# Optimization experiments

Hardware: AMD Instinct MI355X
Metric: run time of the kernel (lower is better)

## Reference

```python
import jax, jax.numpy as jnp
import numpy as np

TINY = 1e-15
EPS = 1e-6
B, T, D, H, N = 1, 512, 512, 8, 64
A = N + 1  # ambient dim
TAU = 1.0


def mink(x, y):
    # Minkowski inner product over the last dim
    return -x[..., 0] * y[..., 0] + jnp.sum(x[..., 1:] * y[..., 1:], axis=-1)


def project(x):
    xx = mink(x, x)
    scale = jnp.sqrt(jnp.maximum(jnp.abs(xx), TINY))[..., None]
    x = x / scale
    return jnp.concatenate([jnp.abs(x[..., :1]), x[..., 1:]], axis=-1)


def exp_map(p, v):
    vn = jnp.sqrt(jnp.maximum(mink(v, v), TINY))[..., None]
    y = jnp.cosh(vn) * p + (jnp.sinh(vn) / jnp.maximum(vn, TINY)) * v
    return project(y)


def log_map(p, y):
    alpha = -mink(p, y)
    dist = jnp.arccosh(jnp.maximum(alpha, 1.0 + EPS))[..., None]
    u = y + alpha[..., None] * p
    un = jnp.sqrt(jnp.maximum(mink(u, u), TINY))[..., None]
    return dist / jnp.maximum(un, TINY) * u


def rope(u):
    # u: [B,H,T,N]; standard half-rotation RoPE, base 10000
    inv_freq = 1.0 / (10000.0 ** (jnp.arange(0, N, 2, dtype=jnp.float32) / N))
    ang = jnp.arange(T, dtype=jnp.float32)[:, None] * inv_freq[None, :]  # [T, N/2]
    cos = jnp.concatenate([jnp.cos(ang), jnp.cos(ang)], axis=-1)  # [T, N]
    sin = jnp.concatenate([jnp.sin(ang), jnp.sin(ang)], axis=-1)
    u1, u2 = u[..., : N // 2], u[..., N // 2:]
    rot = jnp.concatenate([-u2, u1], axis=-1)
    return u * cos + rot * sin


def lift(u):
    # append time-like 0, expmap at origin -> points on hyperboloid [B,H,T,A]
    v = jnp.concatenate([jnp.zeros(u.shape[:-1] + (1,), u.dtype), u], axis=-1)
    o = jnp.zeros((A,), u.dtype).at[0].set(1.0)
    return exp_map(o, v)


def setup_inputs() -> dict:
    key = jax.random.key(0)
    ks = jax.random.split(key, 10)
    s = 0.02
    x = jax.random.normal(ks[0], (B, T, D), jnp.float32)
    Wq = jax.random.normal(ks[1], (D, H * N), jnp.float32) * s
    bq = jax.random.normal(ks[2], (H * N,), jnp.float32) * s
    Wk = jax.random.normal(ks[3], (D, H * N), jnp.float32) * s
    bk = jax.random.normal(ks[4], (H * N,), jnp.float32) * s
    Wv = jax.random.normal(ks[5], (D, H * N), jnp.float32) * s
    bv = jax.random.normal(ks[6], (H * N,), jnp.float32) * s
    Wo = jax.random.normal(ks[7], (H * A, D), jnp.float32) * s
    bo = jax.random.normal(ks[8], (D,), jnp.float32) * s
    sp = jax.random.normal(ks[9], (N,), jnp.float32) * 0.1
    anchor_p = jnp.concatenate([jnp.sqrt(1.0 + jnp.sum(sp * sp))[None], sp])  # valid hyperboloid point
    return dict(x=x, Wq=Wq, bq=bq, Wk=Wk, bk=bk, Wv=Wv, bv=bv, Wo=Wo, bo=bo, anchor_p=anchor_p)


def reference(x, Wq, bq, Wk, bk, Wv, bv, Wo, bo, anchor_p):
    def pack(u):  # [B,T,H*N] -> [B,H,T,N]
        return u.reshape(B, T, H, N).transpose(0, 2, 1, 3)

    uq = rope(pack(x @ Wq + bq))
    uk = rope(pack(x @ Wk + bk))
    uv = pack(x @ Wv + bv)
    Q = lift(uq)  # [B,H,T,A]
    K = lift(uk)
    V = lift(uv)

    # pairwise Lorentz distance scores, softmax in fp32
    alpha_qk = -mink(Q[:, :, :, None, :].astype(jnp.float32), K[:, :, None, :, :].astype(jnp.float32))
    d = jnp.arccosh(jnp.maximum(alpha_qk, 1.0 + EPS))  # [B,H,T,T]
    attn = jax.nn.softmax(-TAU * d * d, axis=-1).astype(V.dtype)

    # one Karcher-mean step around the query point (karcher_steps=1)
    Y = Q
    logv = log_map(Y[:, :, :, None, :], V[:, :, None, :, :])  # [B,H,T,T,A]
    u = jnp.sum(attn[..., None] * logv, axis=3)  # [B,H,T,A]
    Y = exp_map(Y, u)

    Yc = Y.transpose(0, 2, 1, 3)  # [B,T,H,A]
    Z_tan = log_map(anchor_p[None, None, None, :], Yc).reshape(B, T, H * A)
    return Z_tan @ Wo + bo
```

## Files before the change

kernel.cpp:

```cpp
#include <hip/hip_runtime.h>
#include <math.h>

#define T_ 512
#define D_ 512
#define H_ 8
#define N_ 64
#define A_ 65
#define HN_ 512
#define HA_ 520
#define QS_ 66
#define VS_ 66
#define KTS_ 512
#define SYS_ 68
#define EPS_ 1e-6
#define EPSF_ 1e-6f
#define TINY_ 1e-15
#define IT 8
#define PTT 4
#define RPB_ 16
#define BN_ 64
#define CH_ 64
#define NCH_ (D_/CH_)
#define CTT 2

__device__ __forceinline__ double wsumd(double v){
#pragma unroll
  for (int o=32;o;o>>=1) v += __shfl_xor(v,o);
  return v;
}
__device__ __forceinline__ float wsumf(float v){
#pragma unroll
  for (int o=32;o;o>>=1) v += __shfl_xor(v,o);
  return v;
}
__device__ __forceinline__ float wmaxf(float v){
#pragma unroll
  for (int o=32;o;o>>=1) v = fmaxf(v,__shfl_xor(v,o));
  return v;
}
__device__ __forceinline__ float facoshf(float x){
  return __logf(x + sqrtf(fmaf(x,x,-1.f)));
}

__global__ void k_fill(float* __restrict__ out, float val){
  int i = blockIdx.x*256 + threadIdx.x;
  if (i < T_*D_) out[i] = val;
}

__global__ __launch_bounds__(256) void k_trig(double* __restrict__ tab){
  int i = blockIdx.x*256 + threadIdx.x;
  int t = i >> 5, fi = i & 31;
  double inv_f = 1.0 / pow(10000.0, (double)(2*fi)*(1.0/64.0));
  double ang = (double)t * inv_f;
  tab[2*i+0] = cos(ang);
  tab[2*i+1] = sin(ang);
}

__global__ __launch_bounds__(256) void k_projlift(
    const float* __restrict__ x,
    const float* __restrict__ Wq, const float* __restrict__ bq,
    const float* __restrict__ Wk, const float* __restrict__ bk,
    const float* __restrict__ Wv, const float* __restrict__ bv,
    const double* __restrict__ trig,
    float* __restrict__ Qf, float* __restrict__ KTf,
    float* __restrict__ Vf, float* __restrict__ VTf){
  __shared__ float sW[2][CH_*BN_];
  int mode = blockIdx.y;
  const float* W  = (mode==0)?Wq:((mode==1)?Wk:Wv);
  const float* bb = (mode==0)?bq:((mode==1)?bk:bv);
  int tid = threadIdx.x;
  int lane = tid & 63;
  int h = blockIdx.x;
  int n = lane;
  int t0 = __builtin_amdgcn_readfirstlane(blockIdx.z*RPB_ + ((tid>>6)<<2));
  int srr = tid >> 4;
  int scc = (tid*4) & 63;

  float acc[PTT];
#pragma unroll
  for (int i=0;i<PTT;i++) acc[i]=0.f;

  {
    float4 st[4];
#pragma unroll
    for (int k=0;k<4;k++)
      st[k] = *reinterpret_cast<const float4*>(W + (size_t)(k*16+srr)*HN_ + h*BN_ + scc);
#pragma unroll
    for (int k=0;k<4;k++)
      *reinterpret_cast<float4*>(&sW[0][k*1024 + tid*4]) = st[k];
  }
  __syncthreads();

  const float* xr = x + (size_t)t0*D_;
#pragma unroll 1
  for (int ch=0; ch<NCH_; ++ch){
    float4 st[4];
    if (ch+1 < NCH_){
#pragma unroll
      for (int k=0;k<4;k++)
        st[k] = *reinterpret_cast<const float4*>(
            W + (size_t)((ch+1)*CH_ + k*16+srr)*HN_ + h*BN_ + scc);
    }
    const float* sb = &sW[ch&1][0];
    int d0 = ch*CH_;
#pragma unroll 8
    for (int r=0;r<CH_;r++){
      float wd = sb[r*BN_ + lane];
#pragma unroll
      for (int i=0;i<PTT;i++)
        acc[i] = fmaf(xr[(size_t)i*D_ + d0 + r], wd, acc[i]);
    }
    if (ch+1 < NCH_){
#pragma unroll
      for (int k=0;k<4;k++)
        *reinterpret_cast<float4*>(&sW[(ch+1)&1][k*1024 + tid*4]) = st[k];
    }
    __syncthreads();
  }

  float bias = bb[h*BN_ + n];
#pragma unroll 1
  for (int i=0;i<PTT;i++){
    int t = t0 + i;
    double v = (double)(acc[i] + bias);
    if (mode < 2){
      const double2 cs2 = *reinterpret_cast<const double2*>(trig + 2*((size_t)t*32 + (n&31)));
      double vp = __shfl_xor(v, 32);
      double rot = (n<32) ? -vp : vp;
      v = v*cs2.x + rot*cs2.y;
    }
    double ss = wsumd(v*v);
    double vn = sqrt(fmax(ss, TINY_));
    double e  = exp(vn);
    double ei = 1.0/e;
    double ch2 = 0.5*(e+ei);
    double s  = (0.5*(e-ei))/vn;
    double xx = s*s*ss - ch2*ch2;
    double scale = sqrt(fmax(fabs(xx), TINY_));
    float y0 = (float)fabs(ch2/scale);
    float ya = (float)(s*v/scale);
    if (mode==0){
      float* o = Qf + (size_t)h*T_*QS_ + (size_t)t*QS_;
      if (n==0) o[0] = y0;
      o[n+1] = ya;
    } else if (mode==1){
      float* o = KTf + (size_t)h*66*KTS_ + t;
      if (n==0) o[0] = y0;
      o[(size_t)(n+1)*KTS_] = ya;
    } else {
      float* o = Vf + (size_t)h*T_*VS_ + (size_t)t*VS_;
      if (n==0) o[0] = y0;
      o[n+1] = ya;
      float* ot = VTf + (size_t)h*66*KTS_ + t;
      if (n==0) ot[0] = y0;
      ot[(size_t)(n+1)*KTS_] = ya;
    }
  }
}

__global__ __launch_bounds__(256) void k_attnF(
    const float* __restrict__ Qf, const float* __restrict__ KTf,
    const float* __restrict__ VTf, const float* __restrict__ Vf,
    const float* __restrict__ anchor, float* __restrict__ Z){
  __shared__ float  sYf[IT][QS_];
  __shared__ float  sYm[IT][SYS_];
  __shared__ float  s_w[IT][T_];
  __shared__ double sA[A_];
  __shared__ float  s_red[4][IT];
  __shared__ float  s_part[4][IT][64];
  __shared__ float  s_p64[4][IT];

  int h = blockIdx.x, i0 = blockIdx.y*IT, tid = threadIdx.x;
  int wv = tid>>6, lane = tid&63;
  const float* Qp = Qf  + (size_t)h*T_*QS_;
  const float* KT = KTf + (size_t)h*66*KTS_;
  const float* VT = VTf + (size_t)h*66*KTS_;
  const float* Vp = Vf  + (size_t)h*T_*VS_;

  for (int f=tid; f<IT*QS_; f+=256){
    int i=f/QS_, a=f-i*QS_;
    sYf[i][a] = (a<A_) ? Qp[(size_t)(i0+i)*QS_ + a] : 0.f;
  }
  for (int f=tid; f<IT*SYS_; f+=256){
    int i=f/SYS_, a=f-i*SYS_;
    float v = (a<A_) ? Qp[(size_t)(i0+i)*QS_ + a] : 0.f;
    sYm[i][a] = (a==0) ? v : -v;
  }
  if (tid < A_) sA[tid] = (double)anchor[tid];
  __syncthreads();

  int j0 = tid, j1 = tid + 256;
  {
    float aq0[IT], aq1[IT];
#pragma unroll
    for (int i=0;i<IT;i++){ aq0[i]=0.f; aq1[i]=0.f; }
    for (int a4=0; a4<16; a4++){
      int a = a4*4;
      float k00=KT[(size_t)(a+0)*KTS_+j0], k01=KT[(size_t)(a+1)*KTS_+j0];
      float k02=KT[(size_t)(a+2)*KTS_+j0], k03=KT[(size_t)(a+3)*KTS_+j0];
      float k10=KT[(size_t)(a+0)*KTS_+j1], k11=KT[(size_t)(a+1)*KTS_+j1];
      float k12=KT[(size_t)(a+2)*KTS_+j1], k13=KT[(size_t)(a+3)*KTS_+j1];
#pragma unroll
      for (int i=0;i<IT;i++){
        float4 ym = *reinterpret_cast<const float4*>(&sYm[i][a]);
        aq0[i] = fmaf(ym.w,k03,fmaf(ym.z,k02,fmaf(ym.y,k01,fmaf(ym.x,k00,aq0[i]))));
        aq1[i] = fmaf(ym.w,k13,fmaf(ym.z,k12,fmaf(ym.y,k11,fmaf(ym.x,k10,aq1[i]))));
      }
    }
    float kt0 = KT[(size_t)64*KTS_+j0], kt1 = KT[(size_t)64*KTS_+j1];
#pragma unroll
    for (int i=0;i<IT;i++){
      float a0 = fmaf(sYm[i][64], kt0, aq0[i]);
      float a1 = fmaf(sYm[i][64], kt1, aq1[i]);
      float d0 = facoshf(fmaxf(a0, 1.f+EPSF_));
      float d1 = facoshf(fmaxf(a1, 1.f+EPSF_));
      s_w[i][j0] = -d0*d0;
      s_w[i][j1] = -d1*d1;
    }
  }
  __syncthreads();

  for (int ii=0; ii<2; ii++){
    int i = wv*2 + ii;
    float m = -INFINITY;
#pragma unroll
    for (int kk=0;kk<8;kk++) m = fmaxf(m, s_w[i][lane+64*kk]);
    m = wmaxf(m);
    float e[8], sum=0.f;
#pragma unroll
    for (int kk=0;kk<8;kk++){ e[kk]=__expf(s_w[i][lane+64*kk]-m); sum+=e[kk]; }
    sum = wsumf(sum);
    float inv = 1.f/sum;
#pragma unroll
    for (int kk=0;kk<8;kk++) s_w[i][lane+64*kk] = e[kk]*inv;
  }
  __syncthreads();

  {
    float av0[IT], av1[IT];
#pragma unroll
    for (int i=0;i<IT;i++){ av0[i]=0.f; av1[i]=0.f; }
    for (int a4=0; a4<16; a4++){
      int a = a4*4;
      float v00=VT[(size_t)(a+0)*KTS_+j0], v01=VT[(size_t)(a+1)*KTS_+j0];
      float v02=VT[(size_t)(a+2)*KTS_+j0], v03=VT[(size_t)(a+3)*KTS_+j0];
      float v10=VT[(size_t)(a+0)*KTS_+j1], v11=VT[(size_t)(a+1)*KTS_+j1];
      float v12=VT[(size_t)(a+2)*KTS_+j1], v13=VT[(size_t)(a+3)*KTS_+j1];
#pragma unroll
      for (int i=0;i<IT;i++){
        float4 ym = *reinterpret_cast<const float4*>(&sYm[i][a]);
        av0[i] = fmaf(ym.w,v03,fmaf(ym.z,v02,fmaf(ym.y,v01,fmaf(ym.x,v00,av0[i]))));
        av1[i] = fmaf(ym.w,v13,fmaf(ym.z,v12,fmaf(ym.y,v11,fmaf(ym.x,v10,av1[i]))));
      }
    }
    float vt0 = VT[(size_t)64*KTS_+j0], vt1 = VT[(size_t)64*KTS_+j1];
    const float inv_un0 = 3.16227766016838e7f;
    float cyp[IT];
#pragma unroll
    for (int i=0;i<IT;i++){
      float a0 = fmaf(sYm[i][64], vt0, av0[i]);
      float a1 = fmaf(sYm[i][64], vt1, av1[i]);
      float at0 = s_w[i][j0], at1 = s_w[i][j1];
      float d0 = facoshf(fmaxf(a0, 1.f+EPSF_));
      float d1 = facoshf(fmaxf(a1, 1.f+EPSF_));
      float w0 = at0*d0*inv_un0;
      float w1 = at1*d1*inv_un0;
      s_w[i][j0] = w0;
      s_w[i][j1] = w1;
      cyp[i] = fmaf(w0, a0, w1*a1);
    }
#pragma unroll
    for (int i=0;i<IT;i++){
      float r = wsumf(cyp[i]);
      if (lane==0) s_red[wv][i] = r;
    }
  }
  __syncthreads();

  {
    float pL[IT], p64r[IT];
#pragma unroll
    for (int i=0;i<IT;i++){ pL[i]=0.f; p64r[i]=0.f; }
    int jb = wv*128;
    for (int jj=0; jj<128; jj+=4){
      int j = jb + jj;
      float vA = Vp[(size_t)(j+0)*VS_ + lane];
      float vB = Vp[(size_t)(j+1)*VS_ + lane];
      float vC = Vp[(size_t)(j+2)*VS_ + lane];
      float vD = Vp[(size_t)(j+3)*VS_ + lane];
#pragma unroll
      for (int i=0;i<IT;i++){
        float4 w4 = *reinterpret_cast<const float4*>(&s_w[i][j]);
        pL[i] = fmaf(w4.w,vD,fmaf(w4.z,vC,fmaf(w4.y,vB,fmaf(w4.x,vA,pL[i]))));
      }
    }
#pragma unroll
    for (int cc=0; cc<2; cc++){
      int j = jb + cc*64 + lane;
      float v64 = VT[(size_t)64*KTS_ + j];
#pragma unroll
      for (int i=0;i<IT;i++) p64r[i] = fmaf(s_w[i][j], v64, p64r[i]);
    }
#pragma unroll
    for (int i=0;i<IT;i++){
      s_part[wv][i][lane] = pL[i];
      float r = wsumf(p64r[i]);
      if (lane==0) s_p64[wv][i] = r;
    }
  }
  __syncthreads();

  for (int ii=0; ii<2; ii++){
    int r = wv*2 + ii;
    double Yl  = (double)sYf[r][lane];
    double Y64 = (double)sYf[r][64];
    double cy = (double)s_red[0][r]+(double)s_red[1][r]+(double)s_red[2][r]+(double)s_red[3][r];
    double aL = (double)s_part[0][r][lane]+(double)s_part[1][r][lane]
              + (double)s_part[2][r][lane]+(double)s_part[3][r][lane];
    double a64 = (double)s_p64[0][r]+(double)s_p64[1][r]+(double)s_p64[2][r]+(double)s_p64[3][r];
    double ua  = fma(cy, Yl,  aL);
    double u64 = fma(cy, Y64, a64);
    double c2 = (lane==0) ? fma(u64,u64, -ua*ua) : ua*ua;
    double mv = wsumd(c2);
    double vn = sqrt(fmax(mv, TINY_));
    double ch = cosh(vn);
    double sh = sinh(vn)/fmax(vn, TINY_);
    double ya  = fma(ch, Yl,  sh*ua);
    double y64 = fma(ch, Y64, sh*u64);
    double c3 = (lane==0) ? fma(y64,y64, -ya*ya) : ya*ya;
    double px = wsumd(c3);
    double scale = sqrt(fmax(fabs(px), TINY_));
    double Pa  = ya/scale; if (lane==0) Pa = fabs(Pa);
    double P64 = y64/scale;
    double sAl = sA[lane];
    double azc = (lane==0) ? fma(sAl, Pa, -sA[64]*P64) : (-sAl*Pa);
    double az = wsumd(azc);
    double dz = acosh(fmax(az, 1.0+EPS_));
    double uza  = fma(az, sAl,    Pa);
    double uz64 = fma(az, sA[64], P64);
    double c4v = (lane==0) ? fma(uz64,uz64, -uza*uza) : uza*uza;
    double mz = wsumd(c4v);
    double unz = sqrt(fmax(mz, TINY_));
    double fz = dz/fmax(unz, TINY_);
    float* Zr = Z + (size_t)(i0+r)*HA_ + h*A_;
    Zr[lane] = (float)(fz*uza);
    if (lane==0) Zr[64] = (float)(fz*uz64);
  }
}

__global__ __launch_bounds__(256) void k_outD(
    const float* __restrict__ Zb, const float* __restrict__ Wo,
    const float* __restrict__ bo, float* __restrict__ out){
  int c  = blockIdx.x*256 + threadIdx.x;
  int t0 = blockIdx.y*CTT;
  float acc[CTT];
#pragma unroll
  for (int i=0;i<CTT;i++) acc[i]=0.f;
  for (int k=0;k<HA_;k+=4){
    float w0 = Wo[(size_t)(k+0)*D_ + c];
    float w1 = Wo[(size_t)(k+1)*D_ + c];
    float w2 = Wo[(size_t)(k+2)*D_ + c];
    float w3 = Wo[(size_t)(k+3)*D_ + c];
#pragma unroll
    for (int i=0;i<CTT;i++){
      const float* zr = Zb + (size_t)(t0+i)*HA_;
      acc[i] = fmaf(zr[k+0], w0, acc[i]);
      acc[i] = fmaf(zr[k+1], w1, acc[i]);
      acc[i] = fmaf(zr[k+2], w2, acc[i]);
      acc[i] = fmaf(zr[k+3], w3, acc[i]);
    }
  }
  float bb = bo[c];
#pragma unroll
  for (int i=0;i<CTT;i++) out[(t0+i)*D_ + c] = acc[i] + bb;
}

extern "C" void kernel_launch(void* const* d_in, const int* in_sizes, int n_in,
                              void* d_out, int out_size, void* d_ws, size_t ws_size,
                              hipStream_t stream){
  float* out = (float*)d_out;

  bool ok = (n_in == 10) && (out_size == T_*D_)
    && in_sizes[0]==T_*D_ && in_sizes[1]==D_*HN_ && in_sizes[2]==HN_
    && in_sizes[3]==D_*HN_ && in_sizes[4]==HN_
    && in_sizes[5]==D_*HN_ && in_sizes[6]==HN_
    && in_sizes[7]==HA_*D_ && in_sizes[8]==D_ && in_sizes[9]==A_;
  if (!ok){ k_fill<<<1024,256,0,stream>>>(out, 1.0e12f); return; }

  const float* x      = (const float*)d_in[0];
  const float* Wq     = (const float*)d_in[1];
  const float* bq     = (const float*)d_in[2];
  const float* Wk     = (const float*)d_in[3];
  const float* bk     = (const float*)d_in[4];
  const float* Wv     = (const float*)d_in[5];
  const float* bv     = (const float*)d_in[6];
  const float* Wo     = (const float*)d_in[7];
  const float* bo     = (const float*)d_in[8];
  const float* anchor = (const float*)d_in[9];
  char* ws = (char*)d_ws;

  size_t zbytes  = (size_t)T_*HA_*sizeof(float);
  size_t qbytes  = (size_t)H_*T_*QS_*sizeof(float);
  size_t ktbytes = (size_t)H_*66*KTS_*sizeof(float);
  size_t vbytes  = (size_t)H_*T_*VS_*sizeof(float);
  size_t vtbytes = (size_t)H_*66*KTS_*sizeof(float);
  size_t tbytes  = (size_t)T_*32*2*sizeof(double);
  size_t need    = zbytes+qbytes+ktbytes+vbytes+vtbytes+tbytes;
  if (ws_size < need){ k_fill<<<1024,256,0,stream>>>(out, 2.0e12f); return; }

  float*  Zf = (float*)ws;
  float*  Qf = (float*)(ws + zbytes);
  float*  KT = (float*)(ws + zbytes + qbytes);
  float*  Vf = (float*)(ws + zbytes + qbytes + ktbytes);
  float*  VT = (float*)(ws + zbytes + qbytes + ktbytes + vbytes);
  double* TB = (double*)(ws + zbytes + qbytes + ktbytes + vbytes + vtbytes);

  k_trig    <<<dim3(T_*32/256),   256, 0, stream>>>(TB);
  k_projlift<<<dim3(H_,3,T_/RPB_),256, 0, stream>>>(x, Wq,bq, Wk,bk, Wv,bv, TB, Qf, KT, Vf, VT);
  k_attnF   <<<dim3(H_, T_/IT),   256, 0, stream>>>(Qf, KT, VT, Vf, anchor, Zf);
  k_outD    <<<dim3(2, T_/CTT),   256, 0, stream>>>(Zf, Wo, bo, out);
}
```

Measured before the change: 100.3 us.

## Halve attention query tile and vectorize x loads in projection GEMM

```diff
diff --git a/kernel.cpp b/kernel.cpp
--- a/kernel.cpp
+++ b/kernel.cpp
@@ -15,7 +15,7 @@
 #define EPS_ 1e-6
 #define EPSF_ 1e-6f
 #define TINY_ 1e-15
-#define IT 8
+#define IT 4
 #define PTT 4
 #define RPB_ 16
 #define BN_ 64
@@ -72,7 +72,7 @@
   int lane = tid & 63;
   int h = blockIdx.x;
   int n = lane;
-  int t0 = __builtin_amdgcn_readfirstlane(blockIdx.z*RPB_ + ((tid>>6)<<2));
+  int t0 = blockIdx.z*RPB_ + ((tid>>6)<<2);
   int srr = tid >> 4;
   int scc = (tid*4) & 63;
 
@@ -103,12 +103,24 @@
     }
     const float* sb = &sW[ch&1][0];
     int d0 = ch*CH_;
-#pragma unroll 8
-    for (int r=0;r<CH_;r++){
-      float wd = sb[r*BN_ + lane];
+#pragma unroll 4
+    for (int r4=0; r4<CH_/4; r4++){
+      float4 xv[PTT];
 #pragma unroll
       for (int i=0;i<PTT;i++)
-        acc[i] = fmaf(xr[(size_t)i*D_ + d0 + r], wd, acc[i]);
+        xv[i] = *reinterpret_cast<const float4*>(xr + (size_t)i*D_ + d0 + r4*4);
+#pragma unroll
+      for (int j=0;j<4;j++){
+        float wd = sb[(r4*4+j)*BN_ + lane];
+        const float xj0 = (j==0)?xv[0].x:((j==1)?xv[0].y:((j==2)?xv[0].z:xv[0].w));
+        const float xj1 = (j==0)?xv[1].x:((j==1)?xv[1].y:((j==2)?xv[1].z:xv[1].w));
+        const float xj2 = (j==0)?xv[2].x:((j==1)?xv[2].y:((j==2)?xv[2].z:xv[2].w));
+        const float xj3 = (j==0)?xv[3].x:((j==1)?xv[3].y:((j==2)?xv[3].z:xv[3].w));
+        acc[0] = fmaf(xj0, wd, acc[0]);
+        acc[1] = fmaf(xj1, wd, acc[1]);
+        acc[2] = fmaf(xj2, wd, acc[2]);
+        acc[3] = fmaf(xj3, wd, acc[3]);
+      }
     }
     if (ch+1 < NCH_){
 #pragma unroll
@@ -220,8 +232,8 @@
   }
   __syncthreads();
 
-  for (int ii=0; ii<2; ii++){
-    int i = wv*2 + ii;
+  {
+    int i = wv;
     float m = -INFINITY;
 #pragma unroll
     for (int kk=0;kk<8;kk++) m = fmaxf(m, s_w[i][lane+64*kk]);
@@ -310,8 +322,8 @@
   }
   __syncthreads();
 
-  for (int ii=0; ii<2; ii++){
-    int r = wv*2 + ii;
+  {
+    int r = wv;
     double Yl  = (double)sYf[r][lane];
     double Y64 = (double)sYf[r][64];
     double cy = (double)s_red[0][r]+(double)s_red[1][r]+(double)s_red[2][r]+(double)s_red[3][r];
@@ -415,8 +427,8 @@
   float*  VT = (float*)(ws + zbytes + qbytes + ktbytes + vbytes);
   double* TB = (double*)(ws + zbytes + qbytes + ktbytes + vbytes + vtbytes);
 
-  k_trig    <<<dim3(T_*32/256),   256, 0, stream>>>(TB);
-  k_projlift<<<dim3(H_,3,T_/RPB_),256, 0, stream>>>(x, Wq,bq, Wk,bk, Wv,bv, TB, Qf, KT, Vf, VT);
-  k_attnF   <<<dim3(H_, T_/IT),   256, 0, stream>>>(Qf, KT, VT, Vf, anchor, Zf);
-  k_outD    <<<dim3(2, T_/CTT),   256, 0, stream>>>(Zf, Wo, bo, out);
-}
+  k_trig    <<<dim3(T_*32/256),    256, 0, stream>>>(TB);
+  k_projlift<<<dim3(H_,3,T_/RPB_), 256, 0, stream>>>(x, Wq,bq, Wk,bk, Wv,bv, TB, Qf, KT, Vf, VT);
+  k_attnF   <<<dim3(H_, T_/IT),    256, 0, stream>>>(Qf, KT, VT, Vf, anchor, Zf);
+  k_outD    <<<dim3(2, T_/CTT),    256, 0, stream>>>(Zf, Wo, bo, out);
+}
```

Result: slower. 134.2 us (+33.8%).

## Fuse RoPE trig table into projection kernel and halve attention query tile

Applied to the files above, without the earlier changes.

```diff
diff --git a/kernel.cpp b/kernel.cpp
--- a/kernel.cpp
+++ b/kernel.cpp
@@ -15,7 +15,7 @@
 #define EPS_ 1e-6
 #define EPSF_ 1e-6f
 #define TINY_ 1e-15
-#define IT 8
+#define IT 4
 #define PTT 4
 #define RPB_ 16
 #define BN_ 64
@@ -47,24 +47,15 @@
   if (i < T_*D_) out[i] = val;
 }
 
-__global__ __launch_bounds__(256) void k_trig(double* __restrict__ tab){
-  int i = blockIdx.x*256 + threadIdx.x;
-  int t = i >> 5, fi = i & 31;
-  double inv_f = 1.0 / pow(10000.0, (double)(2*fi)*(1.0/64.0));
-  double ang = (double)t * inv_f;
-  tab[2*i+0] = cos(ang);
-  tab[2*i+1] = sin(ang);
-}
-
 __global__ __launch_bounds__(256) void k_projlift(
     const float* __restrict__ x,
     const float* __restrict__ Wq, const float* __restrict__ bq,
     const float* __restrict__ Wk, const float* __restrict__ bk,
     const float* __restrict__ Wv, const float* __restrict__ bv,
-    const double* __restrict__ trig,
     float* __restrict__ Qf, float* __restrict__ KTf,
     float* __restrict__ Vf, float* __restrict__ VTf){
   __shared__ float sW[2][CH_*BN_];
+  __shared__ double2 sTrig[RPB_*32];
   int mode = blockIdx.y;
   const float* W  = (mode==0)?Wq:((mode==1)?Wk:Wv);
   const float* bb = (mode==0)?bq:((mode==1)?bk:bv);
@@ -72,9 +63,21 @@
   int lane = tid & 63;
   int h = blockIdx.x;
   int n = lane;
-  int t0 = __builtin_amdgcn_readfirstlane(blockIdx.z*RPB_ + ((tid>>6)<<2));
+  int t0b = blockIdx.z*RPB_;
+  int t0 = __builtin_amdgcn_readfirstlane(t0b + ((tid>>6)<<2));
   int srr = tid >> 4;
   int scc = (tid*4) & 63;
+
+  if (mode < 2){
+#pragma unroll
+    for (int p=0;p<2;p++){
+      int e = tid + p*256;
+      int lt = e >> 5, fi = e & 31;
+      double inv_f = 1.0 / pow(10000.0, (double)(2*fi)*(1.0/64.0));
+      double ang = (double)(t0b + lt) * inv_f;
+      sTrig[e] = make_double2(cos(ang), sin(ang));
+    }
+  }
 
   float acc[PTT];
 #pragma unroll
@@ -124,7 +127,7 @@
     int t = t0 + i;
     double v = (double)(acc[i] + bias);
     if (mode < 2){
-      const double2 cs2 = *reinterpret_cast<const double2*>(trig + 2*((size_t)t*32 + (n&31)));
+      const double2 cs2 = sTrig[(t - t0b)*32 + (n&31)];
       double vp = __shfl_xor(v, 32);
       double rot = (n<32) ? -vp : vp;
       v = v*cs2.x + rot*cs2.y;
@@ -220,8 +223,8 @@
   }
   __syncthreads();
 
-  for (int ii=0; ii<2; ii++){
-    int i = wv*2 + ii;
+  {
+    int i = wv;
     float m = -INFINITY;
 #pragma unroll
     for (int kk=0;kk<8;kk++) m = fmaxf(m, s_w[i][lane+64*kk]);
@@ -310,8 +313,8 @@
   }
   __syncthreads();
 
-  for (int ii=0; ii<2; ii++){
-    int r = wv*2 + ii;
+  {
+    int r = wv;
     double Yl  = (double)sYf[r][lane];
     double Y64 = (double)sYf[r][64];
     double cy = (double)s_red[0][r]+(double)s_red[1][r]+(double)s_red[2][r]+(double)s_red[3][r];
@@ -404,8 +407,7 @@
   size_t ktbytes = (size_t)H_*66*KTS_*sizeof(float);
   size_t vbytes  = (size_t)H_*T_*VS_*sizeof(float);
   size_t vtbytes = (size_t)H_*66*KTS_*sizeof(float);
-  size_t tbytes  = (size_t)T_*32*2*sizeof(double);
-  size_t need    = zbytes+qbytes+ktbytes+vbytes+vtbytes+tbytes;
+  size_t need    = zbytes+qbytes+ktbytes+vbytes+vtbytes;
   if (ws_size < need){ k_fill<<<1024,256,0,stream>>>(out, 2.0e12f); return; }
 
   float*  Zf = (float*)ws;
@@ -413,10 +415,8 @@
   float*  KT = (float*)(ws + zbytes + qbytes);
   float*  Vf = (float*)(ws + zbytes + qbytes + ktbytes);
   float*  VT = (float*)(ws + zbytes + qbytes + ktbytes + vbytes);
-  double* TB = (double*)(ws + zbytes + qbytes + ktbytes + vbytes + vtbytes);
-
-  k_trig    <<<dim3(T_*32/256),   256, 0, stream>>>(TB);
-  k_projlift<<<dim3(H_,3,T_/RPB_),256, 0, stream>>>(x, Wq,bq, Wk,bk, Wv,bv, TB, Qf, KT, Vf, VT);
-  k_attnF   <<<dim3(H_, T_/IT),   256, 0, stream>>>(Qf, KT, VT, Vf, anchor, Zf);
-  k_outD    <<<dim3(2, T_/CTT),   256, 0, stream>>>(Zf, Wo, bo, out);
-}
+
+  k_projlift<<<dim3(H_,3,T_/RPB_), 256, 0, stream>>>(x, Wq,bq, Wk,bk, Wv,bv, Qf, KT, Vf, VT);
+  k_attnF   <<<dim3(H_, T_/IT),    256, 0, stream>>>(Qf, KT, VT, Vf, anchor, Zf);
+  k_outD    <<<dim3(2, T_/CTT),    256, 0, stream>>>(Zf, Wo, bo, out);
+}
```

Measured after the change: 92.13 us. 1.09x faster.
